# Kernel optimization log

Measured on AMD Instinct MI355X. Metric: run time of the kernel, lower is better.

## Reference

```python
import jax, jax.numpy as jnp
import numpy as np

N = 100000      # nodes
E = 1600000     # edges (avg degree 16)
DIN = 128       # in_feats
H = 4           # num_heads
D = 32          # out_feats per head
NEG_SLOPE = 0.2


def setup_inputs() -> dict:
    key = jax.random.key(0)
    k1, k2, k3, k4, k5, k6 = jax.random.split(key, 6)
    feat = jax.random.normal(k1, (N, DIN), dtype=jnp.float32)
    src = jax.random.randint(k2, (E,), 0, N, dtype=jnp.int32)
    dst = jax.random.randint(k3, (E,), 0, N, dtype=jnp.int32)
    # learned params (fc kernel + attention vectors)
    W = jax.random.normal(k4, (DIN, H * D), dtype=jnp.float32) * 0.05
    attn_l = jax.random.normal(k5, (H, D), dtype=jnp.float32) * 0.05
    attn_r = jax.random.normal(k6, (H, D), dtype=jnp.float32) * 0.05
    return {"feat": feat, "src": src, "dst": dst, "W": W,
            "attn_l": attn_l, "attn_r": attn_r}


def reference(feat, src, dst, W, attn_l, attn_r):
    # linear projection: (N, DIN) @ (DIN, H*D) -> (N, H, D)
    h = (feat @ W).reshape(N, H, D)
    # per-node attention half-logits: (N, H)
    el = jnp.einsum("nhd,hd->nh", h, attn_l)
    er = jnp.einsum("nhd,hd->nh", h, attn_r)
    # edge-wise logits e_ij = LeakyReLU(el[src] + er[dst]) : (E, H)
    e = jax.nn.leaky_relu(el[src] + er[dst], negative_slope=NEG_SLOPE)
    # segment softmax over incoming edges of each dst node
    emax = jax.ops.segment_max(e, dst, num_segments=N)          # (N, H)
    emax = jnp.where(jnp.isfinite(emax), emax, 0.0)             # empty segs
    ee = jnp.exp(e - emax[dst])                                 # (E, H)
    denom = jax.ops.segment_sum(ee, dst, num_segments=N)        # (N, H)
    a = ee / denom[dst]                                         # (E, H)
    # weighted message + scatter-sum aggregation: (N, H, D)
    msg = h[src] * a[:, :, None]                                # (E, H, D)
    out = jax.ops.segment_sum(msg, dst, num_segments=N)
    return out
```

## Files before the change

### kernel.cpp

```cpp
#include <hip/hip_runtime.h>
#include <hip/hip_fp16.h>

#define N_NODES 100000
#define N_EDGES 1600000
#define DIN 128
#define NH 4
#define ND 32
#define HD 128
#define NEG_SLOPE 0.2f
#define MROWS 64
#define APAD 136
#define GEMM_BLOCKS ((N_NODES + MROWS - 1) / MROWS)

#define NBUCK 782
#define CHB 2048
#define NHB 782

typedef _Float16 half8_t __attribute__((ext_vector_type(8)));
typedef float f32x4 __attribute__((ext_vector_type(4)));

__device__ __forceinline__ float lrelu(float x) {
    return x > 0.0f ? x : NEG_SLOPE * x;
}

union Pack8  { uint2 u; __half2 h2[2]; };
union Pack16 { uint4 u; __half2 h2[4]; };

__global__ __launch_bounds__(256) void k_wconv(const float* __restrict__ W,
                                               __half* __restrict__ Wt) {
    int i = blockIdx.x * 256 + threadIdx.x;
    int k = i >> 7, c = i & 127;
    Wt[c * DIN + k] = __float2half(W[k * HD + c]);
}

__global__ __launch_bounds__(256) void k_gemm(
    const float* __restrict__ feat, const __half* __restrict__ Wt,
    const float* __restrict__ attn_l, const float* __restrict__ attn_r,
    __half* __restrict__ hhalf, float* __restrict__ el, float* __restrict__ er) {

    __shared__ __half As[MROWS * APAD];
    __shared__ __half Bs[HD * APAD];

    const int tid = threadIdx.x;
    const int row0 = blockIdx.x * MROWS;

    {
        const uint4* Wv = (const uint4*)Wt;
#pragma unroll
        for (int i = 0; i < 8; ++i) {
            int idx = tid + i * 256;
            int c = idx >> 4, k8 = idx & 15;
            *(uint4*)(&Bs[c * APAD + k8 * 8]) = Wv[idx];
        }
    }
    {
#pragma unroll
        for (int i = 0; i < 8; ++i) {
            int idx = tid + i * 256;
            int r = idx >> 5, c4 = idx & 31;
            int row = row0 + r;
            float4 f = (row < N_NODES)
                ? *(const float4*)(feat + (size_t)row * DIN + c4 * 4)
                : make_float4(0.0f, 0.0f, 0.0f, 0.0f);
            Pack8 pk;
            pk.h2[0] = __floats2half2_rn(f.x, f.y);
            pk.h2[1] = __floats2half2_rn(f.z, f.w);
            *(uint2*)(&As[r * APAD + c4 * 4]) = pk.u;
        }
    }
    __syncthreads();

    const int l = tid & 63;
    const int wv = tid >> 6;
    const int lrow = l & 15;
    const int kid = l >> 4;

    f32x4 acc[8];
#pragma unroll
    for (int n = 0; n < 8; ++n) acc[n] = (f32x4){0.0f, 0.0f, 0.0f, 0.0f};

#pragma unroll
    for (int kb = 0; kb < 4; ++kb) {
        half8_t a = *(const half8_t*)(&As[(wv * 16 + lrow) * APAD + kb * 32 + kid * 8]);
#pragma unroll
        for (int n = 0; n < 8; ++n) {
            half8_t b = *(const half8_t*)(&Bs[(n * 16 + lrow) * APAD + kb * 32 + kid * 8]);
            acc[n] = __builtin_amdgcn_mfma_f32_16x16x32_f16(a, b, acc[n], 0, 0, 0);
        }
    }

    __syncthreads();
#pragma unroll
    for (int n = 0; n < 8; ++n)
#pragma unroll
        for (int r = 0; r < 4; ++r)
            As[(wv * 16 + kid * 4 + r) * APAD + n * 16 + lrow] =
                __float2half(acc[n][r]);
    __syncthreads();

    {
        int lr = tid >> 2;
        int row = row0 + lr;
        int head = tid & 3;
        if (row < N_NODES) {
            float suml = 0.0f, sumr = 0.0f;
#pragma unroll
            for (int q = 0; q < 4; ++q) {
                Pack16 p;
                p.u = *(const uint4*)(&As[lr * APAD + head * 32 + q * 8]);
                float4 al0 = *(const float4*)(attn_l + head * 32 + q * 8);
                float4 al1 = *(const float4*)(attn_l + head * 32 + q * 8 + 4);
                float4 ar0 = *(const float4*)(attn_r + head * 32 + q * 8);
                float4 ar1 = *(const float4*)(attn_r + head * 32 + q * 8 + 4);
                float2 x0 = __half22float2(p.h2[0]);
                float2 x1 = __half22float2(p.h2[1]);
                float2 x2 = __half22float2(p.h2[2]);
                float2 x3 = __half22float2(p.h2[3]);
                suml += x0.x * al0.x + x0.y * al0.y + x1.x * al0.z + x1.y * al0.w;
                suml += x2.x * al1.x + x2.y * al1.y + x3.x * al1.z + x3.y * al1.w;
                sumr += x0.x * ar0.x + x0.y * ar0.y + x1.x * ar0.z + x1.y * ar0.w;
                sumr += x2.x * ar1.x + x2.y * ar1.y + x3.x * ar1.z + x3.y * ar1.w;
                *(uint4*)(hhalf + (size_t)row * HD + head * 32 + q * 8) = p.u;
            }
            el[(size_t)row * NH + head] = suml;
            er[(size_t)row * NH + head] = sumr;
        }
    }
}

__global__ __launch_bounds__(256) void k_hist(const int* __restrict__ dst,
                                              int* __restrict__ hist) {
    __shared__ int cnt[NBUCK];
    int tid = threadIdx.x;
    for (int i = tid; i < NBUCK; i += 256) cnt[i] = 0;
    __syncthreads();
    int base = blockIdx.x * CHB;
#pragma unroll
    for (int j = 0; j < 8; ++j) {
        int e = base + j * 256 + tid;
        if (e < N_EDGES) atomicAdd(&cnt[dst[e] >> 7], 1);
    }
    __syncthreads();
    int* hrow = hist + (size_t)blockIdx.x * NBUCK;
    for (int i = tid; i < NBUCK; i += 256) hrow[i] = cnt[i];
}

__global__ __launch_bounds__(256) void k_scanH(int* __restrict__ hist,
                                               int* __restrict__ tot) {
    __shared__ int wtot[4];
    int b = blockIdx.x, tid = threadIdx.x;
    int idx0 = tid * 4;
    int v[4];
#pragma unroll
    for (int j = 0; j < 4; ++j) {
        int blk = idx0 + j;
        v[j] = (blk < NHB) ? hist[(size_t)blk * NBUCK + b] : 0;
    }
    int s = v[0] + v[1] + v[2] + v[3];
    int lane = tid & 63;
    int incl = s;
#pragma unroll
    for (int off = 1; off < 64; off <<= 1) {
        int t = __shfl_up(incl, off, 64);
        if (lane >= off) incl += t;
    }
    if (lane == 63) wtot[tid >> 6] = incl;
    __syncthreads();
    int woff = 0;
    for (int w = 0; w < (tid >> 6); ++w) woff += wtot[w];
    int run = woff + incl - s;
#pragma unroll
    for (int j = 0; j < 4; ++j) {
        int blk = idx0 + j;
        if (blk < NHB) {
            int old = v[j];
            hist[(size_t)blk * NBUCK + b] = run;
            run += old;
        }
    }
    if (tid == 0) tot[b] = wtot[0] + wtot[1] + wtot[2] + wtot[3];
}

__global__ __launch_bounds__(256) void k_scanT(const int* __restrict__ tot,
                                               int* __restrict__ bucket_base,
                                               int* __restrict__ rowptr) {
    __shared__ int wtot[4];
    int tid = threadIdx.x;
    int idx0 = tid * 4;
    int v[4];
#pragma unroll
    for (int j = 0; j < 4; ++j) {
        int b = idx0 + j;
        v[j] = (b < NBUCK) ? tot[b] : 0;
    }
    int s = v[0] + v[1] + v[2] + v[3];
    int lane = tid & 63;
    int incl = s;
#pragma unroll
    for (int off = 1; off < 64; off <<= 1) {
        int t = __shfl_up(incl, off, 64);
        if (lane >= off) incl += t;
    }
    if (lane == 63) wtot[tid >> 6] = incl;
    __syncthreads();
    int woff = 0;
    for (int w = 0; w < (tid >> 6); ++w) woff += wtot[w];
    int run = woff + incl - s;
#pragma unroll
    for (int j = 0; j < 4; ++j) {
        int b = idx0 + j;
        if (b < NBUCK) {
            int old = v[j];
            bucket_base[b] = run;
            run += old;
        }
    }
    if (tid == 0) {
        int total = wtot[0] + wtot[1] + wtot[2] + wtot[3];
        bucket_base[NBUCK] = total;
        rowptr[N_NODES] = total;
    }
}

__global__ __launch_bounds__(256) void k_cscat(
    const int* __restrict__ src, const int* __restrict__ dst,
    const int* __restrict__ hist, const int* __restrict__ bucket_base,
    int* __restrict__ bucketed) {
    __shared__ int cur[NBUCK];
    int tid = threadIdx.x;
    const int* hrow = hist + (size_t)blockIdx.x * NBUCK;
    for (int i = tid; i < NBUCK; i += 256) cur[i] = bucket_base[i] + hrow[i];
    __syncthreads();
    int base = blockIdx.x * CHB;
#pragma unroll
    for (int j = 0; j < 8; ++j) {
        int e = base + j * 256 + tid;
        if (e < N_EDGES) {
            int d = dst[e];
            int slot = atomicAdd(&cur[d >> 7], 1);
            bucketed[slot] = src[e] | ((d & 127) << 17);
        }
    }
}

__global__ __launch_bounds__(256) void k_fine(
    const int* __restrict__ bucketed, const int* __restrict__ bucket_base,
    int* __restrict__ srcs, int* __restrict__ rowptr) {
    __shared__ int ecnt[128];
    __shared__ int noff[128];
    int b = blockIdx.x, tid = threadIdx.x;
    int beg = bucket_base[b], end = bucket_base[b + 1];
    if (tid < 128) ecnt[tid] = 0;
    __syncthreads();
    for (int e = beg + tid; e < end; e += 256)
        atomicAdd(&ecnt[bucketed[e] >> 17], 1);
    __syncthreads();
    if (tid == 0) {
        int r = 0;
        for (int i = 0; i < 128; ++i) { noff[i] = r; r += ecnt[i]; }
    }
    __syncthreads();
    int nb = b * 128;
    int nn = N_NODES - nb; if (nn > 128) nn = 128;
    if (tid < nn) rowptr[nb + tid] = beg + noff[tid];
    __syncthreads();
    for (int e = beg + tid; e < end; e += 256) {
        int p = bucketed[e];
        int slot = beg + atomicAdd(&noff[p >> 17], 1);
        srcs[slot] = p & 0x1FFFF;
    }
}

__global__ __launch_bounds__(256) void k_agg_csr(
    const int* __restrict__ rowptr, const int* __restrict__ srcs,
    const float* __restrict__ el, const float* __restrict__ er,
    const __half* __restrict__ hhalf, float* __restrict__ out) {
    int node = blockIdx.x * 4 + (threadIdx.x >> 6);
    int lane = threadIdx.x & 63;
    int grp = lane >> 4;
    int cl = lane & 15;
    int head = cl >> 2;
    int beg = rowptr[node], end = rowptr[node + 1];

    const float er_h = er[(size_t)node * NH + head];

    float dsum = 0.0f;
    float a[8];
#pragma unroll
    for (int q = 0; q < 8; ++q) a[q] = 0.0f;

    int i = beg + grp;
    for (; i + 4 < end; i += 8) {
        int s0 = srcs[i];
        int s1 = srcs[i + 4];
        float w0 = __expf(lrelu(el[(size_t)s0 * NH + head] + er_h));
        float w1 = __expf(lrelu(el[(size_t)s1 * NH + head] + er_h));
        Pack16 p0, p1;
        p0.u = *(const uint4*)(hhalf + (size_t)s0 * HD + cl * 8);
        p1.u = *(const uint4*)(hhalf + (size_t)s1 * HD + cl * 8);
        dsum += w0 + w1;
#pragma unroll
        for (int q = 0; q < 4; ++q) {
            float2 x0 = __half22float2(p0.h2[q]);
            float2 x1 = __half22float2(p1.h2[q]);
            a[2 * q]     = fmaf(x0.x, w0, a[2 * q]);
            a[2 * q + 1] = fmaf(x0.y, w0, a[2 * q + 1]);
            a[2 * q]     = fmaf(x1.x, w1, a[2 * q]);
            a[2 * q + 1] = fmaf(x1.y, w1, a[2 * q + 1]);
        }
    }
    if (i < end) {
        int s0 = srcs[i];
        float w0 = __expf(lrelu(el[(size_t)s0 * NH + head] + er_h));
        Pack16 p0;
        p0.u = *(const uint4*)(hhalf + (size_t)s0 * HD + cl * 8);
        dsum += w0;
#pragma unroll
        for (int q = 0; q < 4; ++q) {
            float2 x0 = __half22float2(p0.h2[q]);
            a[2 * q]     = fmaf(x0.x, w0, a[2 * q]);
            a[2 * q + 1] = fmaf(x0.y, w0, a[2 * q + 1]);
        }
    }

    dsum += __shfl_xor(dsum, 16, 64);
    dsum += __shfl_xor(dsum, 32, 64);
#pragma unroll
    for (int q = 0; q < 8; ++q) {
        a[q] += __shfl_xor(a[q], 16, 64);
        a[q] += __shfl_xor(a[q], 32, 64);
    }

    if (grp == 0) {
        float inv = (end > beg) ? 1.0f / dsum : 0.0f;
        *(float4*)(out + (size_t)node * HD + cl * 8) =
            make_float4(a[0] * inv, a[1] * inv, a[2] * inv, a[3] * inv);
        *(float4*)(out + (size_t)node * HD + cl * 8 + 4) =
            make_float4(a[4] * inv, a[5] * inv, a[6] * inv, a[7] * inv);
    }
}

__global__ void k_init_fb(float* __restrict__ out, float* __restrict__ denom) {
    int i = blockIdx.x * blockDim.x + threadIdx.x;
    int stride = gridDim.x * blockDim.x;
    for (int j = i; j < N_NODES * HD; j += stride) out[j] = 0.0f;
    for (int j = i; j < N_NODES * NH; j += stride) denom[j] = 0.0f;
}

__global__ __launch_bounds__(256) void k_denom_fb(
    const int* __restrict__ src, const int* __restrict__ dst,
    const float* __restrict__ el, const float* __restrict__ er,
    float* __restrict__ denom) {
    int e = blockIdx.x * blockDim.x + threadIdx.x;
    if (e >= N_EDGES) return;
    int s = src[e], d = dst[e];
    float4 l = *(const float4*)(el + (size_t)s * NH);
    float4 r = *(const float4*)(er + (size_t)d * NH);
    float* dn = denom + (size_t)d * NH;
    atomicAdd(dn + 0, __expf(lrelu(l.x + r.x)));
    atomicAdd(dn + 1, __expf(lrelu(l.y + r.y)));
    atomicAdd(dn + 2, __expf(lrelu(l.z + r.z)));
    atomicAdd(dn + 3, __expf(lrelu(l.w + r.w)));
}

__global__ __launch_bounds__(256) void k_agg_fb(
    const int* __restrict__ src, const int* __restrict__ dst,
    const float* __restrict__ el, const float* __restrict__ er,
    const float* __restrict__ denom, const __half* __restrict__ hhalf,
    float* __restrict__ out) {
    long long t = (long long)blockIdx.x * blockDim.x + threadIdx.x;
    if (t >= (long long)N_EDGES * HD) return;
    int e = (int)(t >> 7);
    int c = (int)(t & 127);
    int hh = c >> 5;
    int s = src[e], d = dst[e];
    float x = lrelu(el[(size_t)s * NH + hh] + er[(size_t)d * NH + hh]);
    float a = __expf(x) / denom[(size_t)d * NH + hh];
    atomicAdd(out + (size_t)d * HD + c,
              __half2float(hhalf[(size_t)s * HD + c]) * a);
}

extern "C" void kernel_launch(void* const* d_in, const int* in_sizes, int n_in,
                              void* d_out, int out_size, void* d_ws, size_t ws_size,
                              hipStream_t stream) {
    const float* feat   = (const float*)d_in[0];
    const int*   src    = (const int*)d_in[1];
    const int*   dst    = (const int*)d_in[2];
    const float* W      = (const float*)d_in[3];
    const float* attn_l = (const float*)d_in[4];
    const float* attn_r = (const float*)d_in[5];
    float* out = (float*)d_out;

    char* base = (char*)d_ws;
    size_t off = 0;
    auto take = [&](size_t bytes) -> char* {
        char* r = base + off;
        off = (off + bytes + 255) & ~(size_t)255;
        return r;
    };
    __half* hhalf  = (__half*)take((size_t)N_NODES * HD * 2);
    float* el      = (float*)take((size_t)N_NODES * NH * 4);
    float* er      = (float*)take((size_t)N_NODES * NH * 4);
    __half* Wt     = (__half*)take((size_t)DIN * HD * 2);
    int*  hist     = (int*)take((size_t)NHB * NBUCK * 4);
    int*  tot      = (int*)take((size_t)NBUCK * 4);
    int*  bbase    = (int*)take((size_t)(NBUCK + 1) * 4);
    int*  bucketed = (int*)take((size_t)N_EDGES * 4);
    int*  srcs     = (int*)take((size_t)N_EDGES * 4);
    int*  rowptr   = (int*)take((size_t)(N_NODES + 1) * 4);
    float* denom   = (float*)take((size_t)N_NODES * NH * 4);
    bool csr = (off <= ws_size);

    if (csr) {
        k_wconv<<<64, 256, 0, stream>>>(W, Wt);
        k_gemm<<<GEMM_BLOCKS, 256, 0, stream>>>(feat, Wt, attn_l, attn_r,
                                                hhalf, el, er);
        k_hist<<<NHB, 256, 0, stream>>>(dst, hist);
        k_scanH<<<NBUCK, 256, 0, stream>>>(hist, tot);
        k_scanT<<<1, 256, 0, stream>>>(tot, bbase, rowptr);
        k_cscat<<<NHB, 256, 0, stream>>>(src, dst, hist, bbase, bucketed);
        k_fine<<<NBUCK, 256, 0, stream>>>(bucketed, bbase, srcs, rowptr);
        k_agg_csr<<<N_NODES / 4, 256, 0, stream>>>(rowptr, srcs, el, er, hhalf, out);
    } else {
        int eb = (N_EDGES + 255) / 256;
        k_init_fb<<<2048, 256, 0, stream>>>(out, denom);
        k_wconv<<<64, 256, 0, stream>>>(W, Wt);
        k_gemm<<<GEMM_BLOCKS, 256, 0, stream>>>(feat, Wt, attn_l, attn_r,
                                                hhalf, el, er);
        k_denom_fb<<<eb, 256, 0, stream>>>(src, dst, el, er, denom);
        long long totw = (long long)N_EDGES * HD;
        int ab = (int)((totw + 255) / 256);
        k_agg_fb<<<ab, 256, 0, stream>>>(src, dst, el, er, denom, hhalf, out);
    }
}
```

Measured before the change: 170.8 us.

## Fuse histogram into GEMM launch and merge fine sort into LDS-staged aggregation

The dst histogram now runs as extra blocks of the GEMM launch, using larger 8192-edge chunks and a simpler one-value-per-thread scan. The separate fine-sort kernel and CSR arrays are removed. Each aggregation block of 512 threads instead sorts its 128-node bucket in LDS, precomputes per-edge exp weights packed as fp16 together with the softmax denominators, then gathers source features per node. This cuts two launches and the global round trip through srcs and rowptr. In exchange it adds large LDS use per block, fp16 rounding of the edge weights, and a slow fallback path for buckets with more than 2816 edges.

```diff
diff --git a/kernel.cpp b/kernel.cpp
--- a/kernel.cpp
+++ b/kernel.cpp
@@ -13,8 +13,9 @@
 #define GEMM_BLOCKS ((N_NODES + MROWS - 1) / MROWS)
 
 #define NBUCK 782
-#define CHB 2048
-#define NHB 782
+#define CHB 8192
+#define NHB 196
+#define CAP 2816
 
 typedef _Float16 half8_t __attribute__((ext_vector_type(8)));
 typedef float f32x4 __attribute__((ext_vector_type(4)));
@@ -25,6 +26,13 @@
 
 union Pack8  { uint2 u; __half2 h2[2]; };
 union Pack16 { uint4 u; __half2 h2[4]; };
+
+__device__ __forceinline__ float headval(uint2 u, int head) {
+    unsigned x = (head & 2) ? u.y : u.x;
+    x = (head & 1) ? (x >> 16) : (x & 0xFFFFu);
+    __half_raw hr; hr.x = (unsigned short)x;
+    return __half2float((__half)hr);
+}
 
 __global__ __launch_bounds__(256) void k_wconv(const float* __restrict__ W,
                                                __half* __restrict__ Wt) {
@@ -33,15 +41,35 @@
     Wt[c * DIN + k] = __float2half(W[k * HD + c]);
 }
 
-__global__ __launch_bounds__(256) void k_gemm(
+__global__ __launch_bounds__(256) void k_gemmhist(
     const float* __restrict__ feat, const __half* __restrict__ Wt,
     const float* __restrict__ attn_l, const float* __restrict__ attn_r,
-    __half* __restrict__ hhalf, float* __restrict__ el, float* __restrict__ er) {
-
-    __shared__ __half As[MROWS * APAD];
-    __shared__ __half Bs[HD * APAD];
+    __half* __restrict__ hhalf, float* __restrict__ el, float* __restrict__ er,
+    const int* __restrict__ dst, int* __restrict__ hist) {
+
+    __shared__ __align__(16) __half As[MROWS * APAD];
+    __shared__ __align__(16) __half Bs[HD * APAD];
 
     const int tid = threadIdx.x;
+
+    if ((int)blockIdx.x >= GEMM_BLOCKS) {
+        if (!hist) return;
+        int hb = blockIdx.x - GEMM_BLOCKS;
+        int* cnt = (int*)As;
+        for (int i = tid; i < NBUCK; i += 256) cnt[i] = 0;
+        __syncthreads();
+        int base = hb * CHB;
+#pragma unroll
+        for (int j = 0; j < CHB / 256; ++j) {
+            int e = base + j * 256 + tid;
+            if (e < N_EDGES) atomicAdd(&cnt[dst[e] >> 7], 1);
+        }
+        __syncthreads();
+        int* hrow = hist + (size_t)hb * NBUCK;
+        for (int i = tid; i < NBUCK; i += 256) hrow[i] = cnt[i];
+        return;
+    }
+
     const int row0 = blockIdx.x * MROWS;
 
     {
@@ -128,62 +156,28 @@
     }
 }
 
-__global__ __launch_bounds__(256) void k_hist(const int* __restrict__ dst,
-                                              int* __restrict__ hist) {
-    __shared__ int cnt[NBUCK];
-    int tid = threadIdx.x;
-    for (int i = tid; i < NBUCK; i += 256) cnt[i] = 0;
-    __syncthreads();
-    int base = blockIdx.x * CHB;
-#pragma unroll
-    for (int j = 0; j < 8; ++j) {
-        int e = base + j * 256 + tid;
-        if (e < N_EDGES) atomicAdd(&cnt[dst[e] >> 7], 1);
-    }
-    __syncthreads();
-    int* hrow = hist + (size_t)blockIdx.x * NBUCK;
-    for (int i = tid; i < NBUCK; i += 256) hrow[i] = cnt[i];
-}
-
 __global__ __launch_bounds__(256) void k_scanH(int* __restrict__ hist,
                                                int* __restrict__ tot) {
     __shared__ int wtot[4];
     int b = blockIdx.x, tid = threadIdx.x;
-    int idx0 = tid * 4;
-    int v[4];
-#pragma unroll
-    for (int j = 0; j < 4; ++j) {
-        int blk = idx0 + j;
-        v[j] = (blk < NHB) ? hist[(size_t)blk * NBUCK + b] : 0;
-    }
-    int s = v[0] + v[1] + v[2] + v[3];
-    int lane = tid & 63;
-    int incl = s;
+    int v = (tid < NHB) ? hist[(size_t)tid * NBUCK + b] : 0;
+    int lane = tid & 63, wv = tid >> 6;
+    int incl = v;
 #pragma unroll
     for (int off = 1; off < 64; off <<= 1) {
         int t = __shfl_up(incl, off, 64);
         if (lane >= off) incl += t;
     }
-    if (lane == 63) wtot[tid >> 6] = incl;
+    if (lane == 63) wtot[wv] = incl;
     __syncthreads();
     int woff = 0;
-    for (int w = 0; w < (tid >> 6); ++w) woff += wtot[w];
-    int run = woff + incl - s;
-#pragma unroll
-    for (int j = 0; j < 4; ++j) {
-        int blk = idx0 + j;
-        if (blk < NHB) {
-            int old = v[j];
-            hist[(size_t)blk * NBUCK + b] = run;
-            run += old;
-        }
-    }
+    for (int w = 0; w < wv; ++w) woff += wtot[w];
+    if (tid < NHB) hist[(size_t)tid * NBUCK + b] = woff + incl - v;
     if (tid == 0) tot[b] = wtot[0] + wtot[1] + wtot[2] + wtot[3];
 }
 
 __global__ __launch_bounds__(256) void k_scanT(const int* __restrict__ tot,
-                                               int* __restrict__ bucket_base,
-                                               int* __restrict__ rowptr) {
+                                               int* __restrict__ bucket_base) {
     __shared__ int wtot[4];
     int tid = threadIdx.x;
     int idx0 = tid * 4;
@@ -215,11 +209,8 @@
             run += old;
         }
     }
-    if (tid == 0) {
-        int total = wtot[0] + wtot[1] + wtot[2] + wtot[3];
-        bucket_base[NBUCK] = total;
-        rowptr[N_NODES] = total;
-    }
+    if (tid == 0)
+        bucket_base[NBUCK] = wtot[0] + wtot[1] + wtot[2] + wtot[3];
 }
 
 __global__ __launch_bounds__(256) void k_cscat(
@@ -233,7 +224,7 @@
     __syncthreads();
     int base = blockIdx.x * CHB;
 #pragma unroll
-    for (int j = 0; j < 8; ++j) {
+    for (int j = 0; j < CHB / 256; ++j) {
         int e = base + j * 256 + tid;
         if (e < N_EDGES) {
             int d = dst[e];
@@ -243,100 +234,166 @@
     }
 }
 
-__global__ __launch_bounds__(256) void k_fine(
-    const int* __restrict__ bucketed, const int* __restrict__ bucket_base,
-    int* __restrict__ srcs, int* __restrict__ rowptr) {
-    __shared__ int ecnt[128];
-    __shared__ int noff[128];
-    int b = blockIdx.x, tid = threadIdx.x;
-    int beg = bucket_base[b], end = bucket_base[b + 1];
-    if (tid < 128) ecnt[tid] = 0;
-    __syncthreads();
-    for (int e = beg + tid; e < end; e += 256)
-        atomicAdd(&ecnt[bucketed[e] >> 17], 1);
-    __syncthreads();
-    if (tid == 0) {
-        int r = 0;
-        for (int i = 0; i < 128; ++i) { noff[i] = r; r += ecnt[i]; }
-    }
-    __syncthreads();
-    int nb = b * 128;
-    int nn = N_NODES - nb; if (nn > 128) nn = 128;
-    if (tid < nn) rowptr[nb + tid] = beg + noff[tid];
-    __syncthreads();
-    for (int e = beg + tid; e < end; e += 256) {
-        int p = bucketed[e];
-        int slot = beg + atomicAdd(&noff[p >> 17], 1);
-        srcs[slot] = p & 0x1FFFF;
-    }
-}
-
-__global__ __launch_bounds__(256) void k_agg_csr(
-    const int* __restrict__ rowptr, const int* __restrict__ srcs,
+__global__ __launch_bounds__(512) void k_agg(
+    const int* __restrict__ bucketed, const int* __restrict__ bbase,
     const float* __restrict__ el, const float* __restrict__ er,
     const __half* __restrict__ hhalf, float* __restrict__ out) {
-    int node = blockIdx.x * 4 + (threadIdx.x >> 6);
-    int lane = threadIdx.x & 63;
-    int grp = lane >> 4;
-    int cl = lane & 15;
-    int head = cl >> 2;
-    int beg = rowptr[node], end = rowptr[node + 1];
-
-    const float er_h = er[(size_t)node * NH + head];
-
-    float dsum = 0.0f;
-    float a[8];
-#pragma unroll
-    for (int q = 0; q < 8; ++q) a[q] = 0.0f;
-
-    int i = beg + grp;
-    for (; i + 4 < end; i += 8) {
-        int s0 = srcs[i];
-        int s1 = srcs[i + 4];
-        float w0 = __expf(lrelu(el[(size_t)s0 * NH + head] + er_h));
-        float w1 = __expf(lrelu(el[(size_t)s1 * NH + head] + er_h));
-        Pack16 p0, p1;
-        p0.u = *(const uint4*)(hhalf + (size_t)s0 * HD + cl * 8);
-        p1.u = *(const uint4*)(hhalf + (size_t)s1 * HD + cl * 8);
-        dsum += w0 + w1;
-#pragma unroll
-        for (int q = 0; q < 4; ++q) {
-            float2 x0 = __half22float2(p0.h2[q]);
-            float2 x1 = __half22float2(p1.h2[q]);
-            a[2 * q]     = fmaf(x0.x, w0, a[2 * q]);
-            a[2 * q + 1] = fmaf(x0.y, w0, a[2 * q + 1]);
-            a[2 * q]     = fmaf(x1.x, w1, a[2 * q]);
-            a[2 * q + 1] = fmaf(x1.y, w1, a[2 * q + 1]);
-        }
-    }
-    if (i < end) {
-        int s0 = srcs[i];
-        float w0 = __expf(lrelu(el[(size_t)s0 * NH + head] + er_h));
-        Pack16 p0;
-        p0.u = *(const uint4*)(hhalf + (size_t)s0 * HD + cl * 8);
-        dsum += w0;
-#pragma unroll
-        for (int q = 0; q < 4; ++q) {
-            float2 x0 = __half22float2(p0.h2[q]);
-            a[2 * q]     = fmaf(x0.x, w0, a[2 * q]);
-            a[2 * q + 1] = fmaf(x0.y, w0, a[2 * q + 1]);
-        }
-    }
-
-    dsum += __shfl_xor(dsum, 16, 64);
-    dsum += __shfl_xor(dsum, 32, 64);
-#pragma unroll
-    for (int q = 0; q < 8; ++q) {
-        a[q] += __shfl_xor(a[q], 16, 64);
-        a[q] += __shfl_xor(a[q], 32, 64);
-    }
-
-    if (grp == 0) {
-        float inv = (end > beg) ? 1.0f / dsum : 0.0f;
-        *(float4*)(out + (size_t)node * HD + cl * 8) =
-            make_float4(a[0] * inv, a[1] * inv, a[2] * inv, a[3] * inv);
-        *(float4*)(out + (size_t)node * HD + cl * 8 + 4) =
-            make_float4(a[4] * inv, a[5] * inv, a[6] * inv, a[7] * inv);
+
+    __shared__ int s_lds[CAP];
+    __shared__ uint2 w_lds[CAP];
+    __shared__ int cnt[128];
+    __shared__ int noff[129];
+    __shared__ int cur[128];
+    __shared__ float dsum[512];
+    __shared__ float4 er_s[128];
+
+    const int b = blockIdx.x;
+    const int tid = threadIdx.x;
+    const int node0 = b << 7;
+    const int beg = bbase[b], end = bbase[b + 1];
+    const int n = end - beg;
+
+    for (int i = tid; i < 128; i += 512) {
+        cnt[i] = 0;
+        int node = node0 + i;
+        er_s[i] = (node < N_NODES) ? *(const float4*)(er + (size_t)node * NH)
+                                   : make_float4(0.0f, 0.0f, 0.0f, 0.0f);
+    }
+    if (tid < 512) dsum[tid] = 0.0f;
+    __syncthreads();
+
+    const int lane = tid & 63;
+    const int wv = tid >> 6;
+    const int grp = lane >> 4;
+    const int cl = lane & 15;
+    const int head = cl >> 2;
+
+    if (n <= CAP) {
+        for (int e = beg + tid; e < end; e += 512)
+            atomicAdd(&cnt[bucketed[e] >> 17], 1);
+        __syncthreads();
+        if (tid == 0) {
+            int r = 0;
+            for (int i = 0; i < 128; ++i) {
+                noff[i] = r; cur[i] = r; r += cnt[i];
+            }
+            noff[128] = r;
+        }
+        __syncthreads();
+        for (int e = beg + tid; e < end; e += 512) {
+            int p = bucketed[e];
+            int d7 = p >> 17, s = p & 0x1FFFF;
+            int slot = atomicAdd(&cur[d7], 1);
+            s_lds[slot] = s;
+            float4 l = *(const float4*)(el + (size_t)s * NH);
+            float4 r4 = er_s[d7];
+            float w0 = __expf(lrelu(l.x + r4.x));
+            float w1 = __expf(lrelu(l.y + r4.y));
+            float w2 = __expf(lrelu(l.z + r4.z));
+            float w3 = __expf(lrelu(l.w + r4.w));
+            Pack8 pk;
+            pk.h2[0] = __floats2half2_rn(w0, w1);
+            pk.h2[1] = __floats2half2_rn(w2, w3);
+            w_lds[slot] = pk.u;
+            atomicAdd(&dsum[d7 * 4 + 0], w0);
+            atomicAdd(&dsum[d7 * 4 + 1], w1);
+            atomicAdd(&dsum[d7 * 4 + 2], w2);
+            atomicAdd(&dsum[d7 * 4 + 3], w3);
+        }
+        __syncthreads();
+
+        for (int ln = wv; ln < 128; ln += 8) {
+            int node = node0 + ln;
+            if (node >= N_NODES) break;
+            int nb = noff[ln], ne = noff[ln + 1];
+            float a[8];
+#pragma unroll
+            for (int q = 0; q < 8; ++q) a[q] = 0.0f;
+
+            int i = nb + grp;
+            for (; i + 4 < ne; i += 8) {
+                int s0 = s_lds[i], s1 = s_lds[i + 4];
+                float w0 = headval(w_lds[i], head);
+                float w1 = headval(w_lds[i + 4], head);
+                Pack16 p0, p1;
+                p0.u = *(const uint4*)(hhalf + (size_t)s0 * HD + cl * 8);
+                p1.u = *(const uint4*)(hhalf + (size_t)s1 * HD + cl * 8);
+#pragma unroll
+                for (int q = 0; q < 4; ++q) {
+                    float2 x0 = __half22float2(p0.h2[q]);
+                    float2 x1 = __half22float2(p1.h2[q]);
+                    a[2 * q]     = fmaf(x0.x, w0, a[2 * q]);
+                    a[2 * q + 1] = fmaf(x0.y, w0, a[2 * q + 1]);
+                    a[2 * q]     = fmaf(x1.x, w1, a[2 * q]);
+                    a[2 * q + 1] = fmaf(x1.y, w1, a[2 * q + 1]);
+                }
+            }
+            if (i < ne) {
+                int s0 = s_lds[i];
+                float w0 = headval(w_lds[i], head);
+                Pack16 p0;
+                p0.u = *(const uint4*)(hhalf + (size_t)s0 * HD + cl * 8);
+#pragma unroll
+                for (int q = 0; q < 4; ++q) {
+                    float2 x0 = __half22float2(p0.h2[q]);
+                    a[2 * q]     = fmaf(x0.x, w0, a[2 * q]);
+                    a[2 * q + 1] = fmaf(x0.y, w0, a[2 * q + 1]);
+                }
+            }
+#pragma unroll
+            for (int q = 0; q < 8; ++q) {
+                a[q] += __shfl_xor(a[q], 16, 64);
+                a[q] += __shfl_xor(a[q], 32, 64);
+            }
+            if (grp == 0) {
+                float inv = (ne > nb) ? 1.0f / dsum[ln * 4 + head] : 0.0f;
+                *(float4*)(out + (size_t)node * HD + cl * 8) =
+                    make_float4(a[0] * inv, a[1] * inv, a[2] * inv, a[3] * inv);
+                *(float4*)(out + (size_t)node * HD + cl * 8 + 4) =
+                    make_float4(a[4] * inv, a[5] * inv, a[6] * inv, a[7] * inv);
+            }
+        }
+    } else {
+        for (int ln = wv; ln < 128; ln += 8) {
+            int node = node0 + ln;
+            if (node >= N_NODES) break;
+            float4 r4 = er_s[ln];
+            float er_h = (head == 0) ? r4.x : (head == 1) ? r4.y
+                       : (head == 2) ? r4.z : r4.w;
+            float a[8];
+#pragma unroll
+            for (int q = 0; q < 8; ++q) a[q] = 0.0f;
+            float wsum = 0.0f;
+            for (int e = beg + grp; e < end; e += 4) {
+                int p = bucketed[e];
+                if ((p >> 17) != ln) continue;
+                int s = p & 0x1FFFF;
+                float w = __expf(lrelu(el[(size_t)s * NH + head] + er_h));
+                wsum += w;
+                Pack16 p0;
+                p0.u = *(const uint4*)(hhalf + (size_t)s * HD + cl * 8);
+#pragma unroll
+                for (int q = 0; q < 4; ++q) {
+                    float2 x0 = __half22float2(p0.h2[q]);
+                    a[2 * q]     = fmaf(x0.x, w, a[2 * q]);
+                    a[2 * q + 1] = fmaf(x0.y, w, a[2 * q + 1]);
+                }
+            }
+            wsum += __shfl_xor(wsum, 16, 64);
+            wsum += __shfl_xor(wsum, 32, 64);
+#pragma unroll
+            for (int q = 0; q < 8; ++q) {
+                a[q] += __shfl_xor(a[q], 16, 64);
+                a[q] += __shfl_xor(a[q], 32, 64);
+            }
+            if (grp == 0) {
+                float inv = (wsum > 0.0f) ? 1.0f / wsum : 0.0f;
+                *(float4*)(out + (size_t)node * HD + cl * 8) =
+                    make_float4(a[0] * inv, a[1] * inv, a[2] * inv, a[3] * inv);
+                *(float4*)(out + (size_t)node * HD + cl * 8 + 4) =
+                    make_float4(a[4] * inv, a[5] * inv, a[6] * inv, a[7] * inv);
+            }
+        }
     }
 }
 
@@ -406,27 +463,23 @@
     int*  tot      = (int*)take((size_t)NBUCK * 4);
     int*  bbase    = (int*)take((size_t)(NBUCK + 1) * 4);
     int*  bucketed = (int*)take((size_t)N_EDGES * 4);
-    int*  srcs     = (int*)take((size_t)N_EDGES * 4);
-    int*  rowptr   = (int*)take((size_t)(N_NODES + 1) * 4);
     float* denom   = (float*)take((size_t)N_NODES * NH * 4);
     bool csr = (off <= ws_size);
 
     if (csr) {
         k_wconv<<<64, 256, 0, stream>>>(W, Wt);
-        k_gemm<<<GEMM_BLOCKS, 256, 0, stream>>>(feat, Wt, attn_l, attn_r,
-                                                hhalf, el, er);
-        k_hist<<<NHB, 256, 0, stream>>>(dst, hist);
+        k_gemmhist<<<GEMM_BLOCKS + NHB, 256, 0, stream>>>(
+            feat, Wt, attn_l, attn_r, hhalf, el, er, dst, hist);
         k_scanH<<<NBUCK, 256, 0, stream>>>(hist, tot);
-        k_scanT<<<1, 256, 0, stream>>>(tot, bbase, rowptr);
+        k_scanT<<<1, 256, 0, stream>>>(tot, bbase);
         k_cscat<<<NHB, 256, 0, stream>>>(src, dst, hist, bbase, bucketed);
-        k_fine<<<NBUCK, 256, 0, stream>>>(bucketed, bbase, srcs, rowptr);
-        k_agg_csr<<<N_NODES / 4, 256, 0, stream>>>(rowptr, srcs, el, er, hhalf, out);
+        k_agg<<<NBUCK, 512, 0, stream>>>(bucketed, bbase, el, er, hhalf, out);
     } else {
         int eb = (N_EDGES + 255) / 256;
         k_init_fb<<<2048, 256, 0, stream>>>(out, denom);
         k_wconv<<<64, 256, 0, stream>>>(W, Wt);
-        k_gemm<<<GEMM_BLOCKS, 256, 0, stream>>>(feat, Wt, attn_l, attn_r,
-                                                hhalf, el, er);
+        k_gemmhist<<<GEMM_BLOCKS, 256, 0, stream>>>(
+            feat, Wt, attn_l, attn_r, hhalf, el, er, dst, (int*)nullptr);
         k_denom_fb<<<eb, 256, 0, stream>>>(src, dst, el, er, denom);
         long long totw = (long long)N_EDGES * HD;
         int ab = (int)((totw + 255) / 256);
```

Measured after the change: 181.4 us. 1.06x slower.
